# Kernel optimization log

Hardware: AMD Instinct MI355X
Metric: run time of the kernel (lower is better)

## Reference

```python
import jax, jax.numpy as jnp
import numpy as np

N, F, H, C, E = 100000, 64, 128, 10, 1600000
BN_EPS = 1e-5


def setup_inputs() -> dict:
    key = jax.random.key(0)
    ks = jax.random.split(key, 16)
    s = 0.05
    return {
        "x": jax.random.normal(ks[0], (N, F), dtype=jnp.float32),
        "edge_index": jax.random.randint(ks[1], (2, E), 0, N, dtype=jnp.int64),
        # conv1 MLP: Linear(F,H), ReLU, Linear(H,H)
        "w1a": jax.random.normal(ks[2], (F, H), dtype=jnp.float32) * s,
        "b1a": jnp.zeros((H,), jnp.float32),
        "w1b": jax.random.normal(ks[3], (H, H), dtype=jnp.float32) * s,
        "b1b": jnp.zeros((H,), jnp.float32),
        # conv2 MLP: Linear(H,H), ReLU, Linear(H,H)
        "w2a": jax.random.normal(ks[4], (H, H), dtype=jnp.float32) * s,
        "b2a": jnp.zeros((H,), jnp.float32),
        "w2b": jax.random.normal(ks[5], (H, H), dtype=jnp.float32) * s,
        "b2b": jnp.zeros((H,), jnp.float32),
        # BatchNorm affine params
        "bn1_g": jnp.ones((H,), jnp.float32),
        "bn1_b": jnp.zeros((H,), jnp.float32),
        "bn2_g": jnp.ones((H,), jnp.float32),
        "bn2_b": jnp.zeros((H,), jnp.float32),
        # classifier MLP: Linear(H,H), ReLU, (Dropout=identity), Linear(H,C)
        "mw1": jax.random.normal(ks[6], (H, H), dtype=jnp.float32) * s,
        "mb1": jnp.zeros((H,), jnp.float32),
        "mw2": jax.random.normal(ks[7], (H, C), dtype=jnp.float32) * s,
        "mb2": jnp.zeros((C,), jnp.float32),
    }


def _gin_conv(x, src, dst, wa, ba, wb, bb):
    # GINConv, eps=0: mlp( sum_{j in N(i)} x_j + x_i )
    agg = jax.ops.segment_sum(x[src], dst, num_segments=N) + x
    h = jax.nn.relu(agg @ wa + ba)
    return h @ wb + bb


def _batchnorm(h, g, b):
    mean = jnp.mean(h, axis=0)
    var = jnp.var(h, axis=0)  # biased, matches torch BN training normalization
    return (h - mean) * jax.lax.rsqrt(var + BN_EPS) * g + b


def reference(x, edge_index, w1a, b1a, w1b, b1b, w2a, b2a, w2b, b2b,
              bn1_g, bn1_b, bn2_g, bn2_b, mw1, mb1, mw2, mb2):
    src, dst = edge_index[0], edge_index[1]
    h = _gin_conv(x, src, dst, w1a, b1a, w1b, b1b)
    h = jax.nn.relu(_batchnorm(h, bn1_g, bn1_b))
    h = _gin_conv(h, src, dst, w2a, b2a, w2b, b2b)
    latent = jax.nn.relu(_batchnorm(h, bn2_g, bn2_b))
    # classifier (dropout = identity at inference)
    m = jax.nn.relu(latent @ mw1 + mb1)
    class_out = m @ mw2 + mb2
    return latent, class_out
```

## Files before the change

### kernel.cpp

```cpp
#include <hip/hip_runtime.h>
#include <cstdint>


#define NN 100000
#define FF 64
#define HH 128
#define CC 10
#define EE 1600000
#define BN_EPS 1e-5f
#define MBLK 128
#define NBLK_LIN ((NN + MBLK - 1) / MBLK)
#define BSHIFT 7
#define NBUCK ((NN + 127) / 128)
#define CHUNK 16384
#define NB_CH ((EE + CHUNK - 1) / CHUNK)

typedef __attribute__((ext_vector_type(8))) short bf16x8;
typedef __attribute__((ext_vector_type(4))) float f32x4;

__device__ inline unsigned short f2bf(float f) {
    unsigned int u = __float_as_uint(f);
    unsigned int r = (u + 0x7fffu + ((u >> 16) & 1u)) >> 16;
    return (unsigned short)r;
}
__device__ inline float b2f(unsigned short h) {
    return __uint_as_float(((unsigned int)h) << 16);
}
__device__ inline unsigned int pack2(float a, float b) {
    return (unsigned int)f2bf(a) | ((unsigned int)f2bf(b) << 16);
}

__global__ void detect_kernel(const unsigned int* __restrict__ ei, int* __restrict__ flag) {
    if (threadIdx.x == 0) {
        bool i64 = (ei[1] == 0u) && (ei[3] == 0u) && (ei[5] == 0u) && (ei[7] == 0u);
        *flag = i64 ? 1 : 0;
    }
}

__device__ inline int edge_dst(const void* eiv, int f, int e) {
    return f ? (int)((const long long*)eiv)[EE + e] : ((const int*)eiv)[EE + e];
}
__device__ inline int edge_src(const void* eiv, int f, int e) {
    return f ? (int)((const long long*)eiv)[e] : ((const int*)eiv)[e];
}

__global__ __launch_bounds__(256) void p1_hist_kernel(const void* __restrict__ eiv,
                                                      const int* __restrict__ flag,
                                                      int* __restrict__ gbcount) {
    __shared__ int hist[NBUCK];
    const int tid = threadIdx.x;
    const int f = *flag;
    for (int i = tid; i < NBUCK; i += 256) hist[i] = 0;
    __syncthreads();
    int beg = blockIdx.x * CHUNK, end = min(beg + CHUNK, EE);
    for (int e = beg + tid; e < end; e += 256)
        atomicAdd(&hist[edge_dst(eiv, f, e) >> BSHIFT], 1);
    __syncthreads();
    for (int i = tid; i < NBUCK; i += 256)
        if (hist[i]) atomicAdd(&gbcount[i], hist[i]);
}

__global__ __launch_bounds__(1024) void bscan_kernel(const int* __restrict__ gbcount,
                                                     int* __restrict__ gbstart,
                                                     int* __restrict__ gbcursor,
                                                     int* __restrict__ rowstart) {
    __shared__ int s[1024];
    const int tid = threadIdx.x;
    int v = (tid < NBUCK) ? gbcount[tid] : 0;
    s[tid] = v;
    __syncthreads();
    for (int off = 1; off < 1024; off <<= 1) {
        int t = (tid >= off) ? s[tid - off] : 0;
        __syncthreads();
        s[tid] += t;
        __syncthreads();
    }
    if (tid < NBUCK) {
        int e = s[tid] - v;
        gbstart[tid] = e;
        gbcursor[tid] = e;
    }
    if (tid == 0) { gbstart[NBUCK] = EE; rowstart[NN] = EE; }
}

__global__ __launch_bounds__(256) void p2_bin_kernel(const void* __restrict__ eiv,
                                                     const int* __restrict__ flag,
                                                     int* __restrict__ gbcursor,
                                                     unsigned int* __restrict__ packed) {
    __shared__ int hist[NBUCK];
    __shared__ int basep[NBUCK];
    const int tid = threadIdx.x;
    const int f = *flag;
    for (int i = tid; i < NBUCK; i += 256) hist[i] = 0;
    __syncthreads();
    int beg = blockIdx.x * CHUNK, end = min(beg + CHUNK, EE);
    for (int e = beg + tid; e < end; e += 256)
        atomicAdd(&hist[edge_dst(eiv, f, e) >> BSHIFT], 1);
    __syncthreads();
    for (int i = tid; i < NBUCK; i += 256) {
        int c = hist[i];
        if (c) basep[i] = atomicAdd(&gbcursor[i], c);
        hist[i] = 0;
    }
    __syncthreads();
    for (int e = beg + tid; e < end; e += 256) {
        int s = edge_src(eiv, f, e);
        int d = edge_dst(eiv, f, e);
        int b = d >> BSHIFT;
        int r = atomicAdd(&hist[b], 1);
        packed[basep[b] + r] = (unsigned int)s | ((unsigned int)(d & 127) << 17);
    }
}

__global__ __launch_bounds__(256) void p3_sort_kernel(const unsigned int* __restrict__ packed,
                                                      const int* __restrict__ gbstart,
                                                      int* __restrict__ rowstart,
                                                      int* __restrict__ eidx) {
    __shared__ int hist[128];
    __shared__ int excl[128];
    __shared__ int s[128];
    const int tid = threadIdx.x;
    const int b = blockIdx.x;
    const int bstart = gbstart[b], bend = gbstart[b + 1];
    if (tid < 128) hist[tid] = 0;
    __syncthreads();
    for (int e = bstart + tid; e < bend; e += 256)
        atomicAdd(&hist[packed[e] >> 17], 1);
    __syncthreads();
    int v = (tid < 128) ? hist[tid] : 0;
    if (tid < 128) s[tid] = v;
    __syncthreads();
    for (int off = 1; off < 128; off <<= 1) {
        int t = (tid < 128 && tid >= off) ? s[tid - off] : 0;
        __syncthreads();
        if (tid < 128) s[tid] += t;
        __syncthreads();
    }
    if (tid < 128) {
        excl[tid] = s[tid] - v;
        hist[tid] = 0;
        int node = b * 128 + tid;
        if (node < NN) rowstart[node] = bstart + excl[tid];
    }
    __syncthreads();
    for (int e = bstart + tid; e < bend; e += 256) {
        unsigned int p = packed[e];
        int dl = p >> 17;
        int r = atomicAdd(&hist[dl], 1);
        eidx[bstart + excl[dl] + r] = (int)(p & 0x1FFFFu);
    }
}

__global__ __launch_bounds__(256) void cvt_kernel(const float* __restrict__ x,
                                                  unsigned short* __restrict__ xb, int n8) {
    int i = blockIdx.x * 256 + threadIdx.x;
    if (i >= n8) return;
    float4 a = ((const float4*)x)[i * 2];
    float4 b = ((const float4*)x)[i * 2 + 1];
    uint4 o;
    o.x = pack2(a.x, a.y); o.y = pack2(a.z, a.w);
    o.z = pack2(b.x, b.y); o.w = pack2(b.z, b.w);
    ((uint4*)xb)[i] = o;
}

template <int FDIM, int NPB>
__global__ __launch_bounds__(256) void gather_bf_kernel(const unsigned short* __restrict__ xin,
                                                        const int* __restrict__ rowstart,
                                                        const int* __restrict__ eidx,
                                                        unsigned short* __restrict__ agg) {
    constexpr int LPN = FDIM / 2;
    int node = blockIdx.x * NPB + threadIdx.x / LPN;
    int lane = threadIdx.x % LPN;
    if (node >= NN) return;
    int beg = rowstart[node], end = rowstart[node + 1];
    unsigned int self = *(const unsigned int*)(xin + (size_t)node * FDIM + lane * 2);
    float ax = b2f((unsigned short)(self & 0xffff));
    float ay = b2f((unsigned short)(self >> 16));
    int j = beg;
    for (; j + 3 < end; j += 4) {
        int s0 = eidx[j], s1 = eidx[j + 1], s2 = eidx[j + 2], s3 = eidx[j + 3];
        unsigned int v0 = *(const unsigned int*)(xin + (size_t)s0 * FDIM + lane * 2);
        unsigned int v1 = *(const unsigned int*)(xin + (size_t)s1 * FDIM + lane * 2);
        unsigned int v2 = *(const unsigned int*)(xin + (size_t)s2 * FDIM + lane * 2);
        unsigned int v3 = *(const unsigned int*)(xin + (size_t)s3 * FDIM + lane * 2);
        ax += b2f((unsigned short)(v0 & 0xffff)) + b2f((unsigned short)(v1 & 0xffff))
            + b2f((unsigned short)(v2 & 0xffff)) + b2f((unsigned short)(v3 & 0xffff));
        ay += b2f((unsigned short)(v0 >> 16)) + b2f((unsigned short)(v1 >> 16))
            + b2f((unsigned short)(v2 >> 16)) + b2f((unsigned short)(v3 >> 16));
    }
    for (; j < end; j++) {
        unsigned int v0 = *(const unsigned int*)(xin + (size_t)eidx[j] * FDIM + lane * 2);
        ax += b2f((unsigned short)(v0 & 0xffff));
        ay += b2f((unsigned short)(v0 >> 16));
    }
    *(unsigned int*)(agg + (size_t)node * FDIM + lane * 2) = pack2(ax, ay);
}

template <int FDIM, int NPB>
__global__ __launch_bounds__(256) void gather_bn_kernel(const unsigned short* __restrict__ h,
                                                        const int* __restrict__ rowstart,
                                                        const int* __restrict__ eidx,
                                                        const float* __restrict__ a1,
                                                        const float* __restrict__ a0,
                                                        unsigned short* __restrict__ agg) {
    constexpr int LPN = FDIM / 2;
    int node = blockIdx.x * NPB + threadIdx.x / LPN;
    int lane = threadIdx.x % LPN;
    if (node >= NN) return;
    const int c = lane * 2;
    const float s0c = a1[c], s1c = a1[c + 1], o0c = a0[c], o1c = a0[c + 1];
    int beg = rowstart[node], end = rowstart[node + 1];
    unsigned int self = *(const unsigned int*)(h + (size_t)node * FDIM + lane * 2);
    float ax = fmaxf(fmaf(b2f((unsigned short)(self & 0xffff)), s0c, o0c), 0.f);
    float ay = fmaxf(fmaf(b2f((unsigned short)(self >> 16)), s1c, o1c), 0.f);
    int j = beg;
    for (; j + 3 < end; j += 4) {
        int i0 = eidx[j], i1 = eidx[j + 1], i2 = eidx[j + 2], i3 = eidx[j + 3];
        unsigned int v0 = *(const unsigned int*)(h + (size_t)i0 * FDIM + lane * 2);
        unsigned int v1 = *(const unsigned int*)(h + (size_t)i1 * FDIM + lane * 2);
        unsigned int v2 = *(const unsigned int*)(h + (size_t)i2 * FDIM + lane * 2);
        unsigned int v3 = *(const unsigned int*)(h + (size_t)i3 * FDIM + lane * 2);
        ax += fmaxf(fmaf(b2f((unsigned short)(v0 & 0xffff)), s0c, o0c), 0.f)
            + fmaxf(fmaf(b2f((unsigned short)(v1 & 0xffff)), s0c, o0c), 0.f)
            + fmaxf(fmaf(b2f((unsigned short)(v2 & 0xffff)), s0c, o0c), 0.f)
            + fmaxf(fmaf(b2f((unsigned short)(v3 & 0xffff)), s0c, o0c), 0.f);
        ay += fmaxf(fmaf(b2f((unsigned short)(v0 >> 16)), s1c, o1c), 0.f)
            + fmaxf(fmaf(b2f((unsigned short)(v1 >> 16)), s1c, o1c), 0.f)
            + fmaxf(fmaf(b2f((unsigned short)(v2 >> 16)), s1c, o1c), 0.f)
            + fmaxf(fmaf(b2f((unsigned short)(v3 >> 16)), s1c, o1c), 0.f);
    }
    for (; j < end; j++) {
        unsigned int v0 = *(const unsigned int*)(h + (size_t)eidx[j] * FDIM + lane * 2);
        ax += fmaxf(fmaf(b2f((unsigned short)(v0 & 0xffff)), s0c, o0c), 0.f);
        ay += fmaxf(fmaf(b2f((unsigned short)(v0 >> 16)), s1c, o1c), 0.f);
    }
    *(unsigned int*)(agg + (size_t)node * FDIM + lane * 2) = pack2(ax, ay);
}

template <int KIN>
__global__ __launch_bounds__(256) void mlp_kernel(const unsigned short* __restrict__ in,
                                                  const float* __restrict__ Wa,
                                                  const float* __restrict__ ba,
                                                  const float* __restrict__ Wb,
                                                  const float* __restrict__ bb,
                                                  unsigned short* __restrict__ out,
                                                  float* __restrict__ bnsum,
                                                  float* __restrict__ bnsq) {
    constexpr int KLDA = KIN + 8;
    constexpr int CH = KIN / 8;
    __shared__ __attribute__((aligned(16))) unsigned short sA[MBLK * 136];
    __shared__ __attribute__((aligned(16))) unsigned short sW[128 * 136];
    __shared__ float sSt[256];
    __shared__ float sB[256];

    const int tid = threadIdx.x;
    const int wave = tid >> 6, lane = tid & 63;
    const int quad = lane >> 4, l16 = lane & 15;
    const long long row0 = (long long)blockIdx.x * MBLK;

    sSt[tid] = 0.f;
    if (tid < 128) sB[tid] = ba[tid];
    else sB[tid] = bb[tid - 128];

    for (int i = tid; i < KIN * 128; i += 256) {
        int k = i >> 7, n = i & 127;
        sW[n * KLDA + k] = f2bf(Wa[i]);
    }
    for (int i = tid; i < MBLK * CH; i += 256) {
        int r = i / CH, c = i % CH;
        uint4 v = {0u, 0u, 0u, 0u};
        if (row0 + r < NN) v = *(const uint4*)(in + (row0 + r) * KIN + c * 8);
        *(uint4*)(sA + r * KLDA + c * 8) = v;
    }
    __syncthreads();

    f32x4 acc1[2][8];
#pragma unroll
    for (int t = 0; t < 2; t++)
#pragma unroll
        for (int n = 0; n < 8; n++) acc1[t][n] = 0.f;
#pragma unroll
    for (int ks = 0; ks < KIN / 32; ks++) {
        bf16x8 a0 = *(const bf16x8*)(sA + (wave * 32 + l16) * KLDA + ks * 32 + quad * 8);
        bf16x8 a1 = *(const bf16x8*)(sA + (wave * 32 + 16 + l16) * KLDA + ks * 32 + quad * 8);
#pragma unroll
        for (int nt = 0; nt < 8; nt++) {
            bf16x8 b = *(const bf16x8*)(sW + (nt * 16 + l16) * KLDA + ks * 32 + quad * 8);
            acc1[0][nt] = __builtin_amdgcn_mfma_f32_16x16x32_bf16(a0, b, acc1[0][nt], 0, 0, 0);
            acc1[1][nt] = __builtin_amdgcn_mfma_f32_16x16x32_bf16(a1, b, acc1[1][nt], 0, 0, 0);
        }
    }
    __syncthreads();

#pragma unroll
    for (int nt = 0; nt < 8; nt++) {
        const int col = nt * 16 + l16;
        const float bcol = sB[col];
#pragma unroll
        for (int t = 0; t < 2; t++)
#pragma unroll
            for (int r = 0; r < 4; r++) {
                int rl = wave * 32 + t * 16 + quad * 4 + r;
                sA[rl * 136 + col] = f2bf(fmaxf(acc1[t][nt][r] + bcol, 0.f));
            }
    }
    for (int i = tid; i < 128 * 128; i += 256) {
        int k = i >> 7, n = i & 127;
        sW[n * 136 + k] = f2bf(Wb[i]);
    }
    __syncthreads();

    f32x4 acc2[2][8];
#pragma unroll
    for (int t = 0; t < 2; t++)
#pragma unroll
        for (int n = 0; n < 8; n++) acc2[t][n] = 0.f;
#pragma unroll
    for (int ks = 0; ks < 4; ks++) {
        bf16x8 a0 = *(const bf16x8*)(sA + (wave * 32 + l16) * 136 + ks * 32 + quad * 8);
        bf16x8 a1 = *(const bf16x8*)(sA + (wave * 32 + 16 + l16) * 136 + ks * 32 + quad * 8);
#pragma unroll
        for (int nt = 0; nt < 8; nt++) {
            bf16x8 b = *(const bf16x8*)(sW + (nt * 16 + l16) * 136 + ks * 32 + quad * 8);
            acc2[0][nt] = __builtin_amdgcn_mfma_f32_16x16x32_bf16(a0, b, acc2[0][nt], 0, 0, 0);
            acc2[1][nt] = __builtin_amdgcn_mfma_f32_16x16x32_bf16(a1, b, acc2[1][nt], 0, 0, 0);
        }
    }
    __syncthreads();

#pragma unroll
    for (int nt = 0; nt < 8; nt++) {
        const int col = nt * 16 + l16;
        const float bcol = sB[128 + col];
        float ls = 0.f, lq = 0.f;
#pragma unroll
        for (int t = 0; t < 2; t++)
#pragma unroll
            for (int r = 0; r < 4; r++) {
                int rl = wave * 32 + t * 16 + quad * 4 + r;
                float v = acc2[t][nt][r] + bcol;
                if (row0 + rl < NN) { ls += v; lq += v * v; }
                sA[rl * 136 + col] = f2bf(v);
            }
        ls += __shfl_down(ls, 32); ls += __shfl_down(ls, 16);
        lq += __shfl_down(lq, 32); lq += __shfl_down(lq, 16);
        if (lane < 16) { atomicAdd(&sSt[col], ls); atomicAdd(&sSt[128 + col], lq); }
    }
    __syncthreads();

    for (int i = tid; i < MBLK * 16; i += 256) {
        int r = i >> 4, c = i & 15;
        if (row0 + r < NN)
            *(uint4*)(out + (row0 + r) * 128 + c * 8) = *(const uint4*)(sA + r * 136 + c * 8);
    }
    if (tid < 128) atomicAdd(&bnsum[tid], sSt[tid]);
    else atomicAdd(&bnsq[tid - 128], sSt[tid]);
}

__global__ void bn_finalize_kernel(const float* __restrict__ sum, const float* __restrict__ sq,
                                   const float* __restrict__ g, const float* __restrict__ b,
                                   float* __restrict__ a1, float* __restrict__ a0) {
    int c = threadIdx.x;
    if (c < HH) {
        float mean = sum[c] * (1.0f / NN);
        float var = sq[c] * (1.0f / NN) - mean * mean;
        float s = g[c] * rsqrtf(var + BN_EPS);
        a1[c] = s;
        a0[c] = b[c] - mean * s;
    }
}

__global__ __launch_bounds__(256) void final_kernel(const unsigned short* __restrict__ h2,
                                                    const float* __restrict__ a1,
                                                    const float* __restrict__ a0,
                                                    const float* __restrict__ mw1,
                                                    const float* __restrict__ mb1,
                                                    const float* __restrict__ mw2,
                                                    const float* __restrict__ mb2,
                                                    float* __restrict__ latent,
                                                    float* __restrict__ cls) {
    __shared__ __attribute__((aligned(16))) unsigned short sA[MBLK * 136];
    __shared__ __attribute__((aligned(16))) unsigned short sW[128 * 136];
    __shared__ float sBN[256];
    __shared__ float sB1[128];

    const int tid = threadIdx.x;
    const int wave = tid >> 6, lane = tid & 63;
    const int quad = lane >> 4, l16 = lane & 15;
    const long long row0 = (long long)blockIdx.x * MBLK;

    if (tid < 128) { sBN[tid] = a1[tid]; sB1[tid] = mb1[tid]; }
    else sBN[tid] = a0[tid - 128];
    for (int i = tid; i < 128 * 128; i += 256) {
        int k = i >> 7, n = i & 127;
        sW[n * 136 + k] = f2bf(mw1[i]);
    }
    __syncthreads();

    for (int i = tid; i < MBLK * 16; i += 256) {
        int r = i >> 4, c = i & 15;
        bool live = (row0 + r < NN);
        uint4 hv = {0u, 0u, 0u, 0u};
        if (live) hv = *(const uint4*)(h2 + (row0 + r) * 128 + c * 8);
        const unsigned int* wv = (const unsigned int*)&hv;
        float vs[8];
#pragma unroll
        for (int p = 0; p < 4; p++) {
            int cc = c * 8 + p * 2;
            vs[p * 2]     = fmaxf(fmaf(b2f((unsigned short)(wv[p] & 0xffff)), sBN[cc], sBN[128 + cc]), 0.f);
            vs[p * 2 + 1] = fmaxf(fmaf(b2f((unsigned short)(wv[p] >> 16)), sBN[cc + 1], sBN[129 + cc]), 0.f);
        }
        if (live) {
            float4 f0 = {vs[0], vs[1], vs[2], vs[3]};
            float4 f1 = {vs[4], vs[5], vs[6], vs[7]};
            float* lp = latent + (row0 + r) * 128 + c * 8;
            *(float4*)lp = f0;
            *(float4*)(lp + 4) = f1;
        }
        uint4 o;
        o.x = pack2(vs[0], vs[1]); o.y = pack2(vs[2], vs[3]);
        o.z = pack2(vs[4], vs[5]); o.w = pack2(vs[6], vs[7]);
        *(uint4*)(sA + r * 136 + c * 8) = o;
    }
    __syncthreads();

    f32x4 acc1[2][8];
#pragma unroll
    for (int t = 0; t < 2; t++)
#pragma unroll
        for (int n = 0; n < 8; n++) acc1[t][n] = 0.f;
#pragma unroll
    for (int ks = 0; ks < 4; ks++) {
        bf16x8 av0 = *(const bf16x8*)(sA + (wave * 32 + l16) * 136 + ks * 32 + quad * 8);
        bf16x8 av1 = *(const bf16x8*)(sA + (wave * 32 + 16 + l16) * 136 + ks * 32 + quad * 8);
#pragma unroll
        for (int nt = 0; nt < 8; nt++) {
            bf16x8 b = *(const bf16x8*)(sW + (nt * 16 + l16) * 136 + ks * 32 + quad * 8);
            acc1[0][nt] = __builtin_amdgcn_mfma_f32_16x16x32_bf16(av0, b, acc1[0][nt], 0, 0, 0);
            acc1[1][nt] = __builtin_amdgcn_mfma_f32_16x16x32_bf16(av1, b, acc1[1][nt], 0, 0, 0);
        }
    }
    __syncthreads();

#pragma unroll
    for (int nt = 0; nt < 8; nt++) {
        const int col = nt * 16 + l16;
        const float bcol = sB1[col];
#pragma unroll
        for (int t = 0; t < 2; t++)
#pragma unroll
            for (int r = 0; r < 4; r++) {
                int rl = wave * 32 + t * 16 + quad * 4 + r;
                sA[rl * 136 + col] = f2bf(fmaxf(acc1[t][nt][r] + bcol, 0.f));
            }
    }
    for (int i = tid; i < 16 * 128; i += 256) {
        int n = i & 15, k = i >> 4;
        sW[n * 136 + k] = (n < CC) ? f2bf(mw2[k * CC + n]) : (unsigned short)0;
    }
    __syncthreads();

    f32x4 acc2[2];
    acc2[0] = 0.f; acc2[1] = 0.f;
#pragma unroll
    for (int ks = 0; ks < 4; ks++) {
        bf16x8 av0 = *(const bf16x8*)(sA + (wave * 32 + l16) * 136 + ks * 32 + quad * 8);
        bf16x8 av1 = *(const bf16x8*)(sA + (wave * 32 + 16 + l16) * 136 + ks * 32 + quad * 8);
        bf16x8 b = *(const bf16x8*)(sW + l16 * 136 + ks * 32 + quad * 8);
        acc2[0] = __builtin_amdgcn_mfma_f32_16x16x32_bf16(av0, b, acc2[0], 0, 0, 0);
        acc2[1] = __builtin_amdgcn_mfma_f32_16x16x32_bf16(av1, b, acc2[1], 0, 0, 0);
    }
    __syncthreads();

    float* sOf = (float*)sA;
    if (l16 < CC) {
        const float bc = mb2[l16];
#pragma unroll
        for (int t = 0; t < 2; t++)
#pragma unroll
            for (int r = 0; r < 4; r++) {
                int rl = wave * 32 + t * 16 + quad * 4 + r;
                sOf[rl * CC + l16] = acc2[t][r] + bc;
            }
    }
    __syncthreads();
    for (int i = tid; i < MBLK * CC; i += 256) {
        long long gi = row0 * CC + i;
        if (gi < (long long)NN * CC) cls[gi] = sOf[i];
    }
}

extern "C" void kernel_launch(void* const* d_in, const int* in_sizes, int n_in,
                              void* d_out, int out_size, void* d_ws, size_t ws_size,
                              hipStream_t stream) {
    const float* x   = (const float*)d_in[0];
    const void* ei   = d_in[1];
    const float* w1a = (const float*)d_in[2];
    const float* b1a = (const float*)d_in[3];
    const float* w1b = (const float*)d_in[4];
    const float* b1b = (const float*)d_in[5];
    const float* w2a = (const float*)d_in[6];
    const float* b2a = (const float*)d_in[7];
    const float* w2b = (const float*)d_in[8];
    const float* b2b = (const float*)d_in[9];
    const float* bn1g = (const float*)d_in[10];
    const float* bn1b = (const float*)d_in[11];
    const float* bn2g = (const float*)d_in[12];
    const float* bn2b = (const float*)d_in[13];
    const float* mw1 = (const float*)d_in[14];
    const float* mb1 = (const float*)d_in[15];
    const float* mw2 = (const float*)d_in[16];
    const float* mb2 = (const float*)d_in[17];
    float* out = (float*)d_out;

    char* w = (char*)d_ws;
    unsigned short* agg1 = (unsigned short*)w;  w += (size_t)NN * FF * 2;
    unsigned short* h    = (unsigned short*)w;  w += (size_t)NN * HH * 2;
    unsigned short* agg2 = (unsigned short*)w;  w += (size_t)NN * HH * 2;
    unsigned short* xb   = (unsigned short*)w;  w += (size_t)NN * FF * 2;
    float* stats = (float*)w;                   w += 1024 * 4;
    int* eidx = (int*)w;                        w += (size_t)EE * 4;
    unsigned int* packed = (unsigned int*)w;    w += (size_t)EE * 4;
    int* rowstart = (int*)w;                    w += (NN + 2) * 4;
    int* flag = (int*)w;                        w += 16;
    int* gbcount = (int*)w;                     w += (NBUCK + 2) * 4;
    int* gbstart = (int*)w;                     w += (NBUCK + 2) * 4;
    int* gbcursor = (int*)w;                    w += (NBUCK + 2) * 4;

    hipMemsetAsync(stats, 0, 512 * sizeof(float), stream);
    hipMemsetAsync(gbcount, 0, NBUCK * sizeof(int), stream);
    detect_kernel<<<1, 64, 0, stream>>>((const unsigned int*)ei, flag);

    p1_hist_kernel<<<NB_CH, 256, 0, stream>>>(ei, flag, gbcount);
    bscan_kernel<<<1, 1024, 0, stream>>>(gbcount, gbstart, gbcursor, rowstart);
    p2_bin_kernel<<<NB_CH, 256, 0, stream>>>(ei, flag, gbcursor, packed);
    p3_sort_kernel<<<NBUCK, 256, 0, stream>>>(packed, gbstart, rowstart, eidx);

    cvt_kernel<<<(NN * FF / 8 + 255) / 256, 256, 0, stream>>>(x, xb, NN * FF / 8);
    gather_bf_kernel<FF, 8><<<(NN + 7) / 8, 256, 0, stream>>>(xb, rowstart, eidx, agg1);
    mlp_kernel<FF><<<NBLK_LIN, 256, 0, stream>>>(agg1, w1a, b1a, w1b, b1b, h, stats, stats + 128);
    bn_finalize_kernel<<<1, 128, 0, stream>>>(stats, stats + 128, bn1g, bn1b, stats + 512, stats + 640);

    gather_bn_kernel<HH, 4><<<(NN + 3) / 4, 256, 0, stream>>>(h, rowstart, eidx,
                                                              stats + 512, stats + 640, agg2);
    mlp_kernel<HH><<<NBLK_LIN, 256, 0, stream>>>(agg2, w2a, b2a, w2b, b2b, h, stats + 256, stats + 384);
    bn_finalize_kernel<<<1, 128, 0, stream>>>(stats + 256, stats + 384, bn2g, bn2b, stats + 768, stats + 896);

    final_kernel<<<NBLK_LIN, 256, 0, stream>>>(h, stats + 768, stats + 896, mw1, mb1, mw2, mb2,
                                               out, out + (size_t)NN * HH);
}
```

Baseline: 450.0 us.

## Fuse neighbor gather into MLP conv kernels and pre-transpose weights once

The CSR gather-aggregation is merged into the MLP kernel, so each 128-node block gathers its neighbors straight into shared memory and runs both MFMA GEMMs, which removes the agg1/agg2 round trips through global memory. Weights are converted to transposed bf16 once in a combined prep kernel that also zeroes the stats and bucket counters and converts x, replacing two memsets and the cvt kernel. BN finalize is folded into the consumer kernels, and int64 detection is done inline, which removes several small launches. Blocks grow to 512 threads with 16 rows per wave; the gather now shares a block with the GEMM, which may lower latency hiding during the irregular loads.

```diff
diff --git a/kernel.cpp b/kernel.cpp
--- a/kernel.cpp
+++ b/kernel.cpp
@@ -8,12 +8,13 @@
 #define CC 10
 #define EE 1600000
 #define BN_EPS 1e-5f
-#define MBLK 128
-#define NBLK_LIN ((NN + MBLK - 1) / MBLK)
 #define BSHIFT 7
 #define NBUCK ((NN + 127) / 128)
 #define CHUNK 16384
 #define NB_CH ((EE + CHUNK - 1) / CHUNK)
+#define NB_CVT 3125
+#define TW (8192 + 4 * 16384 + 2048)
+#define TWB ((TW + 255) / 256)
 
 typedef __attribute__((ext_vector_type(8))) short bf16x8;
 typedef __attribute__((ext_vector_type(4))) float f32x4;
@@ -29,14 +30,9 @@
 __device__ inline unsigned int pack2(float a, float b) {
     return (unsigned int)f2bf(a) | ((unsigned int)f2bf(b) << 16);
 }
-
-__global__ void detect_kernel(const unsigned int* __restrict__ ei, int* __restrict__ flag) {
-    if (threadIdx.x == 0) {
-        bool i64 = (ei[1] == 0u) && (ei[3] == 0u) && (ei[5] == 0u) && (ei[7] == 0u);
-        *flag = i64 ? 1 : 0;
-    }
-}
-
+__device__ inline int detect_i64(const unsigned int* e) {
+    return (e[1] | e[3] | e[5] | e[7]) == 0u;
+}
 __device__ inline int edge_dst(const void* eiv, int f, int e) {
     return f ? (int)((const long long*)eiv)[EE + e] : ((const int*)eiv)[EE + e];
 }
@@ -44,12 +40,58 @@
     return f ? (int)((const long long*)eiv)[e] : ((const int*)eiv)[e];
 }
 
+__global__ __launch_bounds__(256) void cvtprep_kernel(
+    const float* __restrict__ x, unsigned short* __restrict__ xb,
+    const float* __restrict__ w1a, const float* __restrict__ w1b,
+    const float* __restrict__ w2a, const float* __restrict__ w2b,
+    const float* __restrict__ mw1, const float* __restrict__ mw2,
+    unsigned short* __restrict__ wt1a, unsigned short* __restrict__ wt1b,
+    unsigned short* __restrict__ wt2a, unsigned short* __restrict__ wt2b,
+    unsigned short* __restrict__ wtm1, unsigned short* __restrict__ wtm2,
+    float* __restrict__ stats, int* __restrict__ gbcount) {
+    const int tid = threadIdx.x;
+    const int b = blockIdx.x;
+    if (b == 0) {
+        for (int i = tid; i < 512; i += 256) stats[i] = 0.f;
+        for (int i = tid; i < NBUCK; i += 256) gbcount[i] = 0;
+    }
+    if (b < NB_CVT) {
+        int i = b * 256 + tid;
+        float4 a = ((const float4*)x)[i * 2];
+        float4 c = ((const float4*)x)[i * 2 + 1];
+        uint4 o;
+        o.x = pack2(a.x, a.y); o.y = pack2(a.z, a.w);
+        o.z = pack2(c.x, c.y); o.w = pack2(c.z, c.w);
+        ((uint4*)xb)[i] = o;
+        return;
+    }
+    int idx = (b - NB_CVT) * 256 + tid;
+    if (idx < 8192) {
+        int k = idx >> 7, n = idx & 127;
+        wt1a[n * 64 + k] = f2bf(w1a[idx]);
+    } else if (idx < 8192 + 16384) {
+        int t = idx - 8192; int k = t >> 7, n = t & 127;
+        wt1b[n * 128 + k] = f2bf(w1b[t]);
+    } else if (idx < 8192 + 2 * 16384) {
+        int t = idx - (8192 + 16384); int k = t >> 7, n = t & 127;
+        wt2a[n * 128 + k] = f2bf(w2a[t]);
+    } else if (idx < 8192 + 3 * 16384) {
+        int t = idx - (8192 + 2 * 16384); int k = t >> 7, n = t & 127;
+        wt2b[n * 128 + k] = f2bf(w2b[t]);
+    } else if (idx < 8192 + 4 * 16384) {
+        int t = idx - (8192 + 3 * 16384); int k = t >> 7, n = t & 127;
+        wtm1[n * 128 + k] = f2bf(mw1[t]);
+    } else if (idx < TW) {
+        int t = idx - (8192 + 4 * 16384); int n = t & 15, k = t >> 4;
+        wtm2[n * 128 + k] = (n < CC) ? f2bf(mw2[k * CC + n]) : (unsigned short)0;
+    }
+}
+
 __global__ __launch_bounds__(256) void p1_hist_kernel(const void* __restrict__ eiv,
-                                                      const int* __restrict__ flag,
                                                       int* __restrict__ gbcount) {
     __shared__ int hist[NBUCK];
     const int tid = threadIdx.x;
-    const int f = *flag;
+    const int f = detect_i64((const unsigned int*)eiv);
     for (int i = tid; i < NBUCK; i += 256) hist[i] = 0;
     __syncthreads();
     int beg = blockIdx.x * CHUNK, end = min(beg + CHUNK, EE);
@@ -84,13 +126,12 @@
 }
 
 __global__ __launch_bounds__(256) void p2_bin_kernel(const void* __restrict__ eiv,
-                                                     const int* __restrict__ flag,
                                                      int* __restrict__ gbcursor,
                                                      unsigned int* __restrict__ packed) {
     __shared__ int hist[NBUCK];
     __shared__ int basep[NBUCK];
     const int tid = threadIdx.x;
-    const int f = *flag;
+    const int f = detect_i64((const unsigned int*)eiv);
     for (int i = tid; i < NBUCK; i += 256) hist[i] = 0;
     __syncthreads();
     int beg = blockIdx.x * CHUNK, end = min(beg + CHUNK, EE);
@@ -151,143 +192,99 @@
     }
 }
 
-__global__ __launch_bounds__(256) void cvt_kernel(const float* __restrict__ x,
-                                                  unsigned short* __restrict__ xb, int n8) {
-    int i = blockIdx.x * 256 + threadIdx.x;
-    if (i >= n8) return;
-    float4 a = ((const float4*)x)[i * 2];
-    float4 b = ((const float4*)x)[i * 2 + 1];
-    uint4 o;
-    o.x = pack2(a.x, a.y); o.y = pack2(a.z, a.w);
-    o.z = pack2(b.x, b.y); o.w = pack2(b.z, b.w);
-    ((uint4*)xb)[i] = o;
-}
-
-template <int FDIM, int NPB>
-__global__ __launch_bounds__(256) void gather_bf_kernel(const unsigned short* __restrict__ xin,
-                                                        const int* __restrict__ rowstart,
-                                                        const int* __restrict__ eidx,
-                                                        unsigned short* __restrict__ agg) {
-    constexpr int LPN = FDIM / 2;
-    int node = blockIdx.x * NPB + threadIdx.x / LPN;
-    int lane = threadIdx.x % LPN;
-    if (node >= NN) return;
-    int beg = rowstart[node], end = rowstart[node + 1];
-    unsigned int self = *(const unsigned int*)(xin + (size_t)node * FDIM + lane * 2);
-    float ax = b2f((unsigned short)(self & 0xffff));
-    float ay = b2f((unsigned short)(self >> 16));
-    int j = beg;
-    for (; j + 3 < end; j += 4) {
-        int s0 = eidx[j], s1 = eidx[j + 1], s2 = eidx[j + 2], s3 = eidx[j + 3];
-        unsigned int v0 = *(const unsigned int*)(xin + (size_t)s0 * FDIM + lane * 2);
-        unsigned int v1 = *(const unsigned int*)(xin + (size_t)s1 * FDIM + lane * 2);
-        unsigned int v2 = *(const unsigned int*)(xin + (size_t)s2 * FDIM + lane * 2);
-        unsigned int v3 = *(const unsigned int*)(xin + (size_t)s3 * FDIM + lane * 2);
-        ax += b2f((unsigned short)(v0 & 0xffff)) + b2f((unsigned short)(v1 & 0xffff))
-            + b2f((unsigned short)(v2 & 0xffff)) + b2f((unsigned short)(v3 & 0xffff));
-        ay += b2f((unsigned short)(v0 >> 16)) + b2f((unsigned short)(v1 >> 16))
-            + b2f((unsigned short)(v2 >> 16)) + b2f((unsigned short)(v3 >> 16));
-    }
-    for (; j < end; j++) {
-        unsigned int v0 = *(const unsigned int*)(xin + (size_t)eidx[j] * FDIM + lane * 2);
-        ax += b2f((unsigned short)(v0 & 0xffff));
-        ay += b2f((unsigned short)(v0 >> 16));
-    }
-    *(unsigned int*)(agg + (size_t)node * FDIM + lane * 2) = pack2(ax, ay);
-}
-
-template <int FDIM, int NPB>
-__global__ __launch_bounds__(256) void gather_bn_kernel(const unsigned short* __restrict__ h,
-                                                        const int* __restrict__ rowstart,
-                                                        const int* __restrict__ eidx,
-                                                        const float* __restrict__ a1,
-                                                        const float* __restrict__ a0,
-                                                        unsigned short* __restrict__ agg) {
-    constexpr int LPN = FDIM / 2;
-    int node = blockIdx.x * NPB + threadIdx.x / LPN;
-    int lane = threadIdx.x % LPN;
-    if (node >= NN) return;
-    const int c = lane * 2;
-    const float s0c = a1[c], s1c = a1[c + 1], o0c = a0[c], o1c = a0[c + 1];
-    int beg = rowstart[node], end = rowstart[node + 1];
-    unsigned int self = *(const unsigned int*)(h + (size_t)node * FDIM + lane * 2);
-    float ax = fmaxf(fmaf(b2f((unsigned short)(self & 0xffff)), s0c, o0c), 0.f);
-    float ay = fmaxf(fmaf(b2f((unsigned short)(self >> 16)), s1c, o1c), 0.f);
-    int j = beg;
-    for (; j + 3 < end; j += 4) {
-        int i0 = eidx[j], i1 = eidx[j + 1], i2 = eidx[j + 2], i3 = eidx[j + 3];
-        unsigned int v0 = *(const unsigned int*)(h + (size_t)i0 * FDIM + lane * 2);
-        unsigned int v1 = *(const unsigned int*)(h + (size_t)i1 * FDIM + lane * 2);
-        unsigned int v2 = *(const unsigned int*)(h + (size_t)i2 * FDIM + lane * 2);
-        unsigned int v3 = *(const unsigned int*)(h + (size_t)i3 * FDIM + lane * 2);
-        ax += fmaxf(fmaf(b2f((unsigned short)(v0 & 0xffff)), s0c, o0c), 0.f)
-            + fmaxf(fmaf(b2f((unsigned short)(v1 & 0xffff)), s0c, o0c), 0.f)
-            + fmaxf(fmaf(b2f((unsigned short)(v2 & 0xffff)), s0c, o0c), 0.f)
-            + fmaxf(fmaf(b2f((unsigned short)(v3 & 0xffff)), s0c, o0c), 0.f);
-        ay += fmaxf(fmaf(b2f((unsigned short)(v0 >> 16)), s1c, o1c), 0.f)
-            + fmaxf(fmaf(b2f((unsigned short)(v1 >> 16)), s1c, o1c), 0.f)
-            + fmaxf(fmaf(b2f((unsigned short)(v2 >> 16)), s1c, o1c), 0.f)
-            + fmaxf(fmaf(b2f((unsigned short)(v3 >> 16)), s1c, o1c), 0.f);
-    }
-    for (; j < end; j++) {
-        unsigned int v0 = *(const unsigned int*)(h + (size_t)eidx[j] * FDIM + lane * 2);
-        ax += fmaxf(fmaf(b2f((unsigned short)(v0 & 0xffff)), s0c, o0c), 0.f);
-        ay += fmaxf(fmaf(b2f((unsigned short)(v0 >> 16)), s1c, o1c), 0.f);
-    }
-    *(unsigned int*)(agg + (size_t)node * FDIM + lane * 2) = pack2(ax, ay);
-}
-
-template <int KIN>
-__global__ __launch_bounds__(256) void mlp_kernel(const unsigned short* __restrict__ in,
-                                                  const float* __restrict__ Wa,
-                                                  const float* __restrict__ ba,
-                                                  const float* __restrict__ Wb,
-                                                  const float* __restrict__ bb,
-                                                  unsigned short* __restrict__ out,
-                                                  float* __restrict__ bnsum,
-                                                  float* __restrict__ bnsq) {
+template <int KIN, int BN>
+__global__ __launch_bounds__(512, 4) void conv_kernel(
+    const unsigned short* __restrict__ src,
+    const int* __restrict__ rowstart, const int* __restrict__ eidx,
+    const unsigned short* __restrict__ wTa, const float* __restrict__ ba,
+    const unsigned short* __restrict__ wTb, const float* __restrict__ bb,
+    const float* __restrict__ statsum, const float* __restrict__ statsq,
+    const float* __restrict__ bng, const float* __restrict__ bnb,
+    unsigned short* __restrict__ out,
+    float* __restrict__ bnsum, float* __restrict__ bnsq) {
     constexpr int KLDA = KIN + 8;
     constexpr int CH = KIN / 8;
-    __shared__ __attribute__((aligned(16))) unsigned short sA[MBLK * 136];
+    __shared__ __attribute__((aligned(16))) unsigned short sA[128 * 136];
     __shared__ __attribute__((aligned(16))) unsigned short sW[128 * 136];
+    __shared__ float sBN[256];
+    __shared__ float sB[256];
     __shared__ float sSt[256];
-    __shared__ float sB[256];
-
     const int tid = threadIdx.x;
     const int wave = tid >> 6, lane = tid & 63;
     const int quad = lane >> 4, l16 = lane & 15;
-    const long long row0 = (long long)blockIdx.x * MBLK;
-
-    sSt[tid] = 0.f;
+    const int rt = wave * 16;
+    const int row0 = blockIdx.x * 128;
+
+    if (tid < 256) sSt[tid] = 0.f;
     if (tid < 128) sB[tid] = ba[tid];
-    else sB[tid] = bb[tid - 128];
-
-    for (int i = tid; i < KIN * 128; i += 256) {
-        int k = i >> 7, n = i & 127;
-        sW[n * KLDA + k] = f2bf(Wa[i]);
-    }
-    for (int i = tid; i < MBLK * CH; i += 256) {
-        int r = i / CH, c = i % CH;
-        uint4 v = {0u, 0u, 0u, 0u};
-        if (row0 + r < NN) v = *(const uint4*)(in + (row0 + r) * KIN + c * 8);
-        *(uint4*)(sA + r * KLDA + c * 8) = v;
-    }
-    __syncthreads();
-
-    f32x4 acc1[2][8];
-#pragma unroll
-    for (int t = 0; t < 2; t++)
-#pragma unroll
-        for (int n = 0; n < 8; n++) acc1[t][n] = 0.f;
+    else if (tid < 256) sB[tid] = bb[tid - 128];
+    if (BN && tid < 128) {
+        float mean = statsum[tid] * (1.0f / NN);
+        float var = statsq[tid] * (1.0f / NN) - mean * mean;
+        float sc = bng[tid] * rsqrtf(var + BN_EPS);
+        sBN[tid] = sc;
+        sBN[128 + tid] = bnb[tid] - mean * sc;
+    }
+    for (int i = tid; i < 128 * CH; i += 512)
+        *(uint4*)(sW + (i / CH) * KLDA + (i % CH) * 8) = ((const uint4*)wTa)[i];
+    __syncthreads();
+
+    {
+        constexpr int LPN = KIN / 2;
+        constexpr int NCON = 512 / LPN;
+        const int lane2 = tid % LPN;
+        const int nl0 = tid / LPN;
+        const int c = lane2 * 2;
+        float s0c = 1.f, s1c = 1.f, o0c = 0.f, o1c = 0.f;
+        if (BN) { s0c = sBN[c]; s1c = sBN[c + 1]; o0c = sBN[128 + c]; o1c = sBN[129 + c]; }
+        for (int nl = nl0; nl < 128; nl += NCON) {
+            int node = row0 + nl;
+            float ax = 0.f, ay = 0.f;
+            auto addv = [&](unsigned int v) {
+                float f0 = b2f((unsigned short)(v & 0xffff));
+                float f1 = b2f((unsigned short)(v >> 16));
+                if (BN) {
+                    f0 = fmaxf(fmaf(f0, s0c, o0c), 0.f);
+                    f1 = fmaxf(fmaf(f1, s1c, o1c), 0.f);
+                }
+                ax += f0; ay += f1;
+            };
+            if (node < NN) {
+                addv(*(const unsigned int*)(src + (size_t)node * KIN + c));
+                int beg = rowstart[node], end = rowstart[node + 1];
+                int j = beg;
+                for (; j + 7 < end; j += 8) {
+                    int i0 = eidx[j],     i1 = eidx[j + 1], i2 = eidx[j + 2], i3 = eidx[j + 3];
+                    int i4 = eidx[j + 4], i5 = eidx[j + 5], i6 = eidx[j + 6], i7 = eidx[j + 7];
+                    unsigned int v0 = *(const unsigned int*)(src + (size_t)i0 * KIN + c);
+                    unsigned int v1 = *(const unsigned int*)(src + (size_t)i1 * KIN + c);
+                    unsigned int v2 = *(const unsigned int*)(src + (size_t)i2 * KIN + c);
+                    unsigned int v3 = *(const unsigned int*)(src + (size_t)i3 * KIN + c);
+                    unsigned int v4 = *(const unsigned int*)(src + (size_t)i4 * KIN + c);
+                    unsigned int v5 = *(const unsigned int*)(src + (size_t)i5 * KIN + c);
+                    unsigned int v6 = *(const unsigned int*)(src + (size_t)i6 * KIN + c);
+                    unsigned int v7 = *(const unsigned int*)(src + (size_t)i7 * KIN + c);
+                    addv(v0); addv(v1); addv(v2); addv(v3);
+                    addv(v4); addv(v5); addv(v6); addv(v7);
+                }
+                for (; j < end; j++)
+                    addv(*(const unsigned int*)(src + (size_t)eidx[j] * KIN + c));
+            }
+            *(unsigned int*)(sA + nl * KLDA + c) = pack2(ax, ay);
+        }
+    }
+    __syncthreads();
+
+    f32x4 acc1[8];
+#pragma unroll
+    for (int n = 0; n < 8; n++) acc1[n] = 0.f;
 #pragma unroll
     for (int ks = 0; ks < KIN / 32; ks++) {
-        bf16x8 a0 = *(const bf16x8*)(sA + (wave * 32 + l16) * KLDA + ks * 32 + quad * 8);
-        bf16x8 a1 = *(const bf16x8*)(sA + (wave * 32 + 16 + l16) * KLDA + ks * 32 + quad * 8);
+        bf16x8 a = *(const bf16x8*)(sA + (rt + l16) * KLDA + ks * 32 + quad * 8);
 #pragma unroll
         for (int nt = 0; nt < 8; nt++) {
             bf16x8 b = *(const bf16x8*)(sW + (nt * 16 + l16) * KLDA + ks * 32 + quad * 8);
-            acc1[0][nt] = __builtin_amdgcn_mfma_f32_16x16x32_bf16(a0, b, acc1[0][nt], 0, 0, 0);
-            acc1[1][nt] = __builtin_amdgcn_mfma_f32_16x16x32_bf16(a1, b, acc1[1][nt], 0, 0, 0);
+            acc1[nt] = __builtin_amdgcn_mfma_f32_16x16x32_bf16(a, b, acc1[nt], 0, 0, 0);
         }
     }
     __syncthreads();
@@ -297,33 +294,25 @@
         const int col = nt * 16 + l16;
         const float bcol = sB[col];
 #pragma unroll
-        for (int t = 0; t < 2; t++)
-#pragma unroll
-            for (int r = 0; r < 4; r++) {
-                int rl = wave * 32 + t * 16 + quad * 4 + r;
-                sA[rl * 136 + col] = f2bf(fmaxf(acc1[t][nt][r] + bcol, 0.f));
-            }
-    }
-    for (int i = tid; i < 128 * 128; i += 256) {
-        int k = i >> 7, n = i & 127;
-        sW[n * 136 + k] = f2bf(Wb[i]);
-    }
-    __syncthreads();
-
-    f32x4 acc2[2][8];
-#pragma unroll
-    for (int t = 0; t < 2; t++)
-#pragma unroll
-        for (int n = 0; n < 8; n++) acc2[t][n] = 0.f;
+        for (int r = 0; r < 4; r++) {
+            int rl = rt + quad * 4 + r;
+            sA[rl * 136 + col] = f2bf(fmaxf(acc1[nt][r] + bcol, 0.f));
+        }
+    }
+    for (int i = tid; i < 128 * 16; i += 512)
+        *(uint4*)(sW + (i >> 4) * 136 + (i & 15) * 8) = ((const uint4*)wTb)[i];
+    __syncthreads();
+
+    f32x4 acc2[8];
+#pragma unroll
+    for (int n = 0; n < 8; n++) acc2[n] = 0.f;
 #pragma unroll
     for (int ks = 0; ks < 4; ks++) {
-        bf16x8 a0 = *(const bf16x8*)(sA + (wave * 32 + l16) * 136 + ks * 32 + quad * 8);
-        bf16x8 a1 = *(const bf16x8*)(sA + (wave * 32 + 16 + l16) * 136 + ks * 32 + quad * 8);
+        bf16x8 a = *(const bf16x8*)(sA + (rt + l16) * 136 + ks * 32 + quad * 8);
 #pragma unroll
         for (int nt = 0; nt < 8; nt++) {
             bf16x8 b = *(const bf16x8*)(sW + (nt * 16 + l16) * 136 + ks * 32 + quad * 8);
-            acc2[0][nt] = __builtin_amdgcn_mfma_f32_16x16x32_bf16(a0, b, acc2[0][nt], 0, 0, 0);
-            acc2[1][nt] = __builtin_amdgcn_mfma_f32_16x16x32_bf16(a1, b, acc2[1][nt], 0, 0, 0);
+            acc2[nt] = __builtin_amdgcn_mfma_f32_16x16x32_bf16(a, b, acc2[nt], 0, 0, 0);
         }
     }
     __syncthreads();
@@ -334,74 +323,60 @@
         const float bcol = sB[128 + col];
         float ls = 0.f, lq = 0.f;
 #pragma unroll
-        for (int t = 0; t < 2; t++)
-#pragma unroll
-            for (int r = 0; r < 4; r++) {
-                int rl = wave * 32 + t * 16 + quad * 4 + r;
-                float v = acc2[t][nt][r] + bcol;
-                if (row0 + rl < NN) { ls += v; lq += v * v; }
-                sA[rl * 136 + col] = f2bf(v);
-            }
+        for (int r = 0; r < 4; r++) {
+            int rl = rt + quad * 4 + r;
+            float v = acc2[nt][r] + bcol;
+            if (row0 + rl < NN) { ls += v; lq += v * v; }
+            sA[rl * 136 + col] = f2bf(v);
+        }
         ls += __shfl_down(ls, 32); ls += __shfl_down(ls, 16);
         lq += __shfl_down(lq, 32); lq += __shfl_down(lq, 16);
         if (lane < 16) { atomicAdd(&sSt[col], ls); atomicAdd(&sSt[128 + col], lq); }
     }
     __syncthreads();
-
-    for (int i = tid; i < MBLK * 16; i += 256) {
-        int r = i >> 4, c = i & 15;
+    for (int i = tid; i < 128 * 16; i += 512) {
+        int r = i >> 4, cc = i & 15;
         if (row0 + r < NN)
-            *(uint4*)(out + (row0 + r) * 128 + c * 8) = *(const uint4*)(sA + r * 136 + c * 8);
+            *(uint4*)(out + (size_t)(row0 + r) * 128 + cc * 8) = *(const uint4*)(sA + r * 136 + cc * 8);
     }
     if (tid < 128) atomicAdd(&bnsum[tid], sSt[tid]);
-    else atomicAdd(&bnsq[tid - 128], sSt[tid]);
-}
-
-__global__ void bn_finalize_kernel(const float* __restrict__ sum, const float* __restrict__ sq,
-                                   const float* __restrict__ g, const float* __restrict__ b,
-                                   float* __restrict__ a1, float* __restrict__ a0) {
-    int c = threadIdx.x;
-    if (c < HH) {
-        float mean = sum[c] * (1.0f / NN);
-        float var = sq[c] * (1.0f / NN) - mean * mean;
-        float s = g[c] * rsqrtf(var + BN_EPS);
-        a1[c] = s;
-        a0[c] = b[c] - mean * s;
-    }
-}
-
-__global__ __launch_bounds__(256) void final_kernel(const unsigned short* __restrict__ h2,
-                                                    const float* __restrict__ a1,
-                                                    const float* __restrict__ a0,
-                                                    const float* __restrict__ mw1,
-                                                    const float* __restrict__ mb1,
-                                                    const float* __restrict__ mw2,
-                                                    const float* __restrict__ mb2,
-                                                    float* __restrict__ latent,
-                                                    float* __restrict__ cls) {
-    __shared__ __attribute__((aligned(16))) unsigned short sA[MBLK * 136];
+    else if (tid < 256) atomicAdd(&bnsq[tid - 128], sSt[tid]);
+}
+
+__global__ __launch_bounds__(512, 4) void final_kernel(
+    const unsigned short* __restrict__ h2,
+    const float* __restrict__ statsum, const float* __restrict__ statsq,
+    const float* __restrict__ bng, const float* __restrict__ bnb,
+    const unsigned short* __restrict__ wTm1, const float* __restrict__ mb1,
+    const unsigned short* __restrict__ wTm2, const float* __restrict__ mb2,
+    float* __restrict__ latent, float* __restrict__ cls) {
+    __shared__ __attribute__((aligned(16))) unsigned short sA[128 * 136];
     __shared__ __attribute__((aligned(16))) unsigned short sW[128 * 136];
     __shared__ float sBN[256];
     __shared__ float sB1[128];
-
     const int tid = threadIdx.x;
     const int wave = tid >> 6, lane = tid & 63;
     const int quad = lane >> 4, l16 = lane & 15;
-    const long long row0 = (long long)blockIdx.x * MBLK;
-
-    if (tid < 128) { sBN[tid] = a1[tid]; sB1[tid] = mb1[tid]; }
-    else sBN[tid] = a0[tid - 128];
-    for (int i = tid; i < 128 * 128; i += 256) {
-        int k = i >> 7, n = i & 127;
-        sW[n * 136 + k] = f2bf(mw1[i]);
-    }
-    __syncthreads();
-
-    for (int i = tid; i < MBLK * 16; i += 256) {
+    const int rt = wave * 16;
+    const int row0 = blockIdx.x * 128;
+
+    if (tid < 128) {
+        float mean = statsum[tid] * (1.0f / NN);
+        float var = statsq[tid] * (1.0f / NN) - mean * mean;
+        float sc = bng[tid] * rsqrtf(var + BN_EPS);
+        sBN[tid] = sc;
+        sBN[128 + tid] = bnb[tid] - mean * sc;
+        sB1[tid] = mb1[tid];
+    }
+    for (int i = tid; i < 128 * 16; i += 512)
+        *(uint4*)(sW + (i >> 4) * 136 + (i & 15) * 8) = ((const uint4*)wTm1)[i];
+    __syncthreads();
+
+    for (int i = tid; i < 128 * 16; i += 512) {
         int r = i >> 4, c = i & 15;
         bool live = (row0 + r < NN);
         uint4 hv = {0u, 0u, 0u, 0u};
-        if (live) hv = *(const uint4*)(h2 + (row0 + r) * 128 + c * 8);
+        if (live) hv = *(const uint4*)(h2 + (size_t)(row0 + r) * 128 + c * 8);
         const unsigned int* wv = (const unsigned int*)&hv;
         float vs[8];
 #pragma unroll
@@ -413,7 +388,7 @@
         if (live) {
             float4 f0 = {vs[0], vs[1], vs[2], vs[3]};
             float4 f1 = {vs[4], vs[5], vs[6], vs[7]};
-            float* lp = latent + (row0 + r) * 128 + c * 8;
+            float* lp = latent + (size_t)(row0 + r) * 128 + c * 8;
             *(float4*)lp = f0;
             *(float4*)(lp + 4) = f1;
         }
@@ -424,20 +399,16 @@
     }
     __syncthreads();
 
-    f32x4 acc1[2][8];
-#pragma unroll
-    for (int t = 0; t < 2; t++)
-#pragma unroll
-        for (int n = 0; n < 8; n++) acc1[t][n] = 0.f;
+    f32x4 acc1[8];
+#pragma unroll
+    for (int n = 0; n < 8; n++) acc1[n] = 0.f;
 #pragma unroll
     for (int ks = 0; ks < 4; ks++) {
-        bf16x8 av0 = *(const bf16x8*)(sA + (wave * 32 + l16) * 136 + ks * 32 + quad * 8);
-        bf16x8 av1 = *(const bf16x8*)(sA + (wave * 32 + 16 + l16) * 136 + ks * 32 + quad * 8);
+        bf16x8 a = *(const bf16x8*)(sA + (rt + l16) * 136 + ks * 32 + quad * 8);
 #pragma unroll
         for (int nt = 0; nt < 8; nt++) {
             bf16x8 b = *(const bf16x8*)(sW + (nt * 16 + l16) * 136 + ks * 32 + quad * 8);
-            acc1[0][nt] = __builtin_amdgcn_mfma_f32_16x16x32_bf16(av0, b, acc1[0][nt], 0, 0, 0);
-            acc1[1][nt] = __builtin_amdgcn_mfma_f32_16x16x32_bf16(av1, b, acc1[1][nt], 0, 0, 0);
+            acc1[nt] = __builtin_amdgcn_mfma_f32_16x16x32_bf16(a, b, acc1[nt], 0, 0, 0);
         }
     }
     __syncthreads();
@@ -447,28 +418,21 @@
         const int col = nt * 16 + l16;
         const float bcol = sB1[col];
 #pragma unroll
-        for (int t = 0; t < 2; t++)
-#pragma unroll
-            for (int r = 0; r < 4; r++) {
-                int rl = wave * 32 + t * 16 + quad * 4 + r;
-                sA[rl * 136 + col] = f2bf(fmaxf(acc1[t][nt][r] + bcol, 0.f));
-            }
-    }
-    for (int i = tid; i < 16 * 128; i += 256) {
-        int n = i & 15, k = i >> 4;
-        sW[n * 136 + k] = (n < CC) ? f2bf(mw2[k * CC + n]) : (unsigned short)0;
-    }
-    __syncthreads();
-
-    f32x4 acc2[2];
-    acc2[0] = 0.f; acc2[1] = 0.f;
+        for (int r = 0; r < 4; r++) {
+            int rl = rt + quad * 4 + r;
+            sA[rl * 136 + col] = f2bf(fmaxf(acc1[nt][r] + bcol, 0.f));
+        }
+    }
+    if (tid < 256)
+        *(uint4*)(sW + (tid >> 4) * 136 + (tid & 15) * 8) = ((const uint4*)wTm2)[tid];
+    __syncthreads();
+
+    f32x4 acc2 = 0.f;
 #pragma unroll
     for (int ks = 0; ks < 4; ks++) {
-        bf16x8 av0 = *(const bf16x8*)(sA + (wave * 32 + l16) * 136 + ks * 32 + quad * 8);
-        bf16x8 av1 = *(const bf16x8*)(sA + (wave * 32 + 16 + l16) * 136 + ks * 32 + quad * 8);
+        bf16x8 a = *(const bf16x8*)(sA + (rt + l16) * 136 + ks * 32 + quad * 8);
         bf16x8 b = *(const bf16x8*)(sW + l16 * 136 + ks * 32 + quad * 8);
-        acc2[0] = __builtin_amdgcn_mfma_f32_16x16x32_bf16(av0, b, acc2[0], 0, 0, 0);
-        acc2[1] = __builtin_amdgcn_mfma_f32_16x16x32_bf16(av1, b, acc2[1], 0, 0, 0);
+        acc2 = __builtin_amdgcn_mfma_f32_16x16x32_bf16(a, b, acc2, 0, 0, 0);
     }
     __syncthreads();
 
@@ -476,17 +440,15 @@
     if (l16 < CC) {
         const float bc = mb2[l16];
 #pragma unroll
-        for (int t = 0; t < 2; t++)
-#pragma unroll
-            for (int r = 0; r < 4; r++) {
-                int rl = wave * 32 + t * 16 + quad * 4 + r;
-                sOf[rl * CC + l16] = acc2[t][r] + bc;
-            }
-    }
-    __syncthreads();
-    for (int i = tid; i < MBLK * CC; i += 256) {
-        long long gi = row0 * CC + i;
-        if (gi < (long long)NN * CC) cls[gi] = sOf[i];
+        for (int r = 0; r < 4; r++) {
+            int rl = rt + quad * 4 + r;
+            sOf[rl * CC + l16] = acc2[r] + bc;
+        }
+    }
+    __syncthreads();
+    for (int i = tid; i < 128 * CC; i += 512) {
+        int r = i / CC;
+        if (row0 + r < NN) cls[(size_t)(row0 + r) * CC + (i % CC)] = sOf[i];
     }
 }
 
@@ -514,38 +476,41 @@
     float* out = (float*)d_out;
 
     char* w = (char*)d_ws;
-    unsigned short* agg1 = (unsigned short*)w;  w += (size_t)NN * FF * 2;
-    unsigned short* h    = (unsigned short*)w;  w += (size_t)NN * HH * 2;
-    unsigned short* agg2 = (unsigned short*)w;  w += (size_t)NN * HH * 2;
-    unsigned short* xb   = (unsigned short*)w;  w += (size_t)NN * FF * 2;
+    unsigned short* xb = (unsigned short*)w;    w += (size_t)NN * FF * 2;
+    unsigned short* h1 = (unsigned short*)w;    w += (size_t)NN * HH * 2;
+    unsigned short* h2 = (unsigned short*)w;    w += (size_t)NN * HH * 2;
     float* stats = (float*)w;                   w += 1024 * 4;
     int* eidx = (int*)w;                        w += (size_t)EE * 4;
     unsigned int* packed = (unsigned int*)w;    w += (size_t)EE * 4;
     int* rowstart = (int*)w;                    w += (NN + 2) * 4;
-    int* flag = (int*)w;                        w += 16;
     int* gbcount = (int*)w;                     w += (NBUCK + 2) * 4;
     int* gbstart = (int*)w;                     w += (NBUCK + 2) * 4;
     int* gbcursor = (int*)w;                    w += (NBUCK + 2) * 4;
-
-    hipMemsetAsync(stats, 0, 512 * sizeof(float), stream);
-    hipMemsetAsync(gbcount, 0, NBUCK * sizeof(int), stream);
-    detect_kernel<<<1, 64, 0, stream>>>((const unsigned int*)ei, flag);
-
-    p1_hist_kernel<<<NB_CH, 256, 0, stream>>>(ei, flag, gbcount);
+    unsigned short* wt1a = (unsigned short*)w;  w += 8192 * 2;
+    unsigned short* wt1b = (unsigned short*)w;  w += 16384 * 2;
+    unsigned short* wt2a = (unsigned short*)w;  w += 16384 * 2;
+    unsigned short* wt2b = (unsigned short*)w;  w += 16384 * 2;
+    unsigned short* wtm1 = (unsigned short*)w;  w += 16384 * 2;
+    unsigned short* wtm2 = (unsigned short*)w;  w += 2048 * 2;
+
+    cvtprep_kernel<<<NB_CVT + TWB, 256, 0, stream>>>(
+        x, xb, w1a, w1b, w2a, w2b, mw1, mw2,
+        wt1a, wt1b, wt2a, wt2b, wtm1, wtm2, stats, gbcount);
+
+    p1_hist_kernel<<<NB_CH, 256, 0, stream>>>(ei, gbcount);
     bscan_kernel<<<1, 1024, 0, stream>>>(gbcount, gbstart, gbcursor, rowstart);
-    p2_bin_kernel<<<NB_CH, 256, 0, stream>>>(ei, flag, gbcursor, packed);
+    p2_bin_kernel<<<NB_CH, 256, 0, stream>>>(ei, gbcursor, packed);
     p3_sort_kernel<<<NBUCK, 256, 0, stream>>>(packed, gbstart, rowstart, eidx);
 
-    cvt_kernel<<<(NN * FF / 8 + 255) / 256, 256, 0, stream>>>(x, xb, NN * FF / 8);
-    gather_bf_kernel<FF, 8><<<(NN + 7) / 8, 256, 0, stream>>>(xb, rowstart, eidx, agg1);
-    mlp_kernel<FF><<<NBLK_LIN, 256, 0, stream>>>(agg1, w1a, b1a, w1b, b1b, h, stats, stats + 128);
-    bn_finalize_kernel<<<1, 128, 0, stream>>>(stats, stats + 128, bn1g, bn1b, stats + 512, stats + 640);
-
-    gather_bn_kernel<HH, 4><<<(NN + 3) / 4, 256, 0, stream>>>(h, rowstart, eidx,
-                                                              stats + 512, stats + 640, agg2);
-    mlp_kernel<HH><<<NBLK_LIN, 256, 0, stream>>>(agg2, w2a, b2a, w2b, b2b, h, stats + 256, stats + 384);
-    bn_finalize_kernel<<<1, 128, 0, stream>>>(stats + 256, stats + 384, bn2g, bn2b, stats + 768, stats + 896);
-
-    final_kernel<<<NBLK_LIN, 256, 0, stream>>>(h, stats + 768, stats + 896, mw1, mb1, mw2, mb2,
-                                               out, out + (size_t)NN * HH);
-}
+    conv_kernel<FF, 0><<<NBUCK, 512, 0, stream>>>(
+        xb, rowstart, eidx, wt1a, b1a, wt1b, b1b,
+        nullptr, nullptr, nullptr, nullptr, h1, stats, stats + 128);
+
+    conv_kernel<HH, 1><<<NBUCK, 512, 0, stream>>>(
+        h1, rowstart, eidx, wt2a, b2a, wt2b, b2b,
+        stats, stats + 128, bn1g, bn1b, h2, stats + 256, stats + 384);
+
+    final_kernel<<<NBUCK, 512, 0, stream>>>(
+        h2, stats + 256, stats + 384, bn2g, bn2b,
+        wtm1, mb1, wtm2, mb2, out, out + (size_t)NN * HH);
+}
```

Measured after the change: 479.4 us. +6.5%, slower.
